# Kernel optimization log

Measured on AMD Instinct MI355X. Metric: run time of the kernel, lower is better.

The kernel has to match this reference:

```python
import jax, jax.numpy as jnp
import numpy as np

B = 256
H, W = 8, 16          # input_resolution for channels=256
C = 768               # dim = channels*3
WS = 4                # window_size
SHIFT = 2             # shift_size
NH = 12               # num_heads
HD = C // NH          # head_dim = 64
HID = 1024            # mlp hidden = channels*4
N = WS * WS           # tokens per window = 16
NW = (H // WS) * (W // WS)  # windows per image = 8
LN_EPS = 1e-5


def _rel_pos_index():
    coords = np.stack(np.meshgrid(np.arange(WS), np.arange(WS), indexing='ij'))  # [2,ws,ws]
    cf = coords.reshape(2, -1)                      # [2, N]
    rel = (cf[:, :, None] - cf[:, None, :]).transpose(1, 2, 0)  # [N, N, 2]
    rel[:, :, 0] += WS - 1
    rel[:, :, 1] += WS - 1
    rel[:, :, 0] *= 2 * WS - 1
    return jnp.asarray(rel.sum(-1))                 # [N, N] int


def _attn_mask():
    img = np.zeros((H, W))
    slices = (slice(0, -WS), slice(-WS, -SHIFT), slice(-SHIFT, None))
    cnt = 0
    for hs in slices:
        for ws_ in slices:
            img[hs, ws_] = cnt
            cnt += 1
    mw = img.reshape(H // WS, WS, W // WS, WS).transpose(0, 2, 1, 3).reshape(-1, N)  # [nW, N]
    am = mw[:, None, :] - mw[:, :, None]            # [nW, N, N]
    return jnp.asarray(np.where(am != 0, -100.0, 0.0).astype(np.float32))


REL_IDX = _rel_pos_index()
ATTN_MASK = _attn_mask()


def _ln(x, g, b):
    m = x.mean(-1, keepdims=True)
    v = ((x - m) ** 2).mean(-1, keepdims=True)
    return (x - m) / jnp.sqrt(v + LN_EPS) * g + b


def setup_inputs() -> dict:
    key = jax.random.key(0)
    ks = jax.random.split(key, 8)
    s = 0.02
    return {
        'x': jax.random.normal(ks[0], (B, H * W, C), jnp.float32),
        'ln1_g': jnp.ones((C,), jnp.float32),
        'ln1_b': jnp.zeros((C,), jnp.float32),
        'qkv_w': jax.random.normal(ks[1], (C, 3 * C), jnp.float32) * s,
        'qkv_b': jnp.zeros((3 * C,), jnp.float32),
        'proj_w': jax.random.normal(ks[2], (C, C), jnp.float32) * s,
        'proj_b': jnp.zeros((C,), jnp.float32),
        'rel_table': jax.random.normal(ks[3], ((2 * WS - 1) * (2 * WS - 1), NH), jnp.float32) * s,
        'ln2_g': jnp.ones((C,), jnp.float32),
        'ln2_b': jnp.zeros((C,), jnp.float32),
        'fc1_w': jax.random.normal(ks[4], (C, HID), jnp.float32) * s,
        'fc1_b': jax.random.normal(ks[5], (HID,), jnp.float32) * 1e-6,
        'fc2_w': jax.random.normal(ks[6], (HID, C), jnp.float32) * s,
        'fc2_b': jax.random.normal(ks[7], (C,), jnp.float32) * 1e-6,
    }


def reference(x, ln1_g, ln1_b, qkv_w, qkv_b, proj_w, proj_b, rel_table,
              ln2_g, ln2_b, fc1_w, fc1_b, fc2_w, fc2_b):
    # --- norm1 + cyclic shift + window partition ---
    h = _ln(x, ln1_g, ln1_b).reshape(B, H, W, C)
    h = jnp.roll(h, (-SHIFT, -SHIFT), axis=(1, 2))
    hw = h.reshape(B, H // WS, WS, W // WS, WS, C).transpose(0, 1, 3, 2, 4, 5)
    hw = hw.reshape(B * NW, N, C)                   # (num_windows*B, N, C)
    # --- window attention with relative position bias + shift mask ---
    qkv = (hw @ qkv_w + qkv_b).reshape(B * NW, N, 3, NH, HD).transpose(2, 0, 3, 1, 4)
    q, k, v = qkv[0] * (HD ** -0.5), qkv[1], qkv[2]  # [Bn, NH, N, HD]
    attn = jnp.einsum('bhnd,bhmd->bhnm', q, k)      # [Bn, NH, N, N]
    bias = rel_table[REL_IDX].transpose(2, 0, 1)    # [NH, N, N]
    attn = attn + bias[None]
    attn = attn.reshape(B, NW, NH, N, N) + ATTN_MASK[None, :, None]
    attn = jax.nn.softmax(attn.reshape(B * NW, NH, N, N), axis=-1)
    o = jnp.einsum('bhnm,bhmd->bhnd', attn, v).transpose(0, 2, 1, 3).reshape(B * NW, N, C)
    o = o @ proj_w + proj_b
    # --- window reverse + reverse shift + residual ---
    o = o.reshape(B, H // WS, W // WS, WS, WS, C).transpose(0, 1, 3, 2, 4, 5).reshape(B, H, W, C)
    o = jnp.roll(o, (SHIFT, SHIFT), axis=(1, 2)).reshape(B, H * W, C)
    x = x + o
    # --- MLP block (dropout is identity at inference) ---
    y = _ln(x, ln2_g, ln2_b)
    y = jax.nn.gelu(y @ fc1_w + fc1_b, approximate=False)
    return x + (y @ fc2_w + fc2_b)
```

## Files before the change

### kernel.cpp

```cpp
#include <hip/hip_runtime.h>
#include <stdint.h>
#include <stddef.h>

typedef __attribute__((ext_vector_type(8))) short bf16x8;
typedef __attribute__((ext_vector_type(4))) float f32x4;
typedef __attribute__((ext_vector_type(4))) unsigned int uint4v;

static __device__ __forceinline__ unsigned short f2bf(float f) {
  unsigned int u = __builtin_bit_cast(unsigned int, f);
  unsigned int r = (u + 0x7FFFu + ((u >> 16) & 1u)) >> 16;
  return (unsigned short)r;
}
static __device__ __forceinline__ float bf2f(unsigned short h) {
  unsigned int u = ((unsigned int)h) << 16;
  return __builtin_bit_cast(float, u);
}
static __device__ __forceinline__ unsigned int pk2(float a, float b) {
  return (unsigned int)f2bf(a) | ((unsigned int)f2bf(b) << 16);
}

static __device__ __forceinline__ void gld16(const void* g, void* l) {
  __builtin_amdgcn_global_load_lds(
      (const __attribute__((address_space(1))) void*)g,
      (__attribute__((address_space(3))) void*)l, 16, 0, 0);
}

__global__ void transpose_cast_all(const float* __restrict__ s0, unsigned short* __restrict__ d0,
                                   const float* __restrict__ s1, unsigned short* __restrict__ d1,
                                   const float* __restrict__ s2, unsigned short* __restrict__ d2,
                                   const float* __restrict__ s3, unsigned short* __restrict__ d3) {
  __shared__ float tile[32][33];
  const int b = blockIdx.x;
  const float* src; unsigned short* dst; int R, C, nbx, bi;
  if (b < 1728)      { src = s0; dst = d0; R = 768;  C = 2304; nbx = 72; bi = b; }
  else if (b < 2304) { src = s1; dst = d1; R = 768;  C = 768;  nbx = 24; bi = b - 1728; }
  else if (b < 3072) { src = s2; dst = d2; R = 768;  C = 1024; nbx = 32; bi = b - 2304; }
  else               { src = s3; dst = d3; R = 1024; C = 768;  nbx = 24; bi = b - 3072; }
  const int bx = bi % nbx, by = bi / nbx;
  const int c0 = bx * 32, r0 = by * 32;
  const int tx = threadIdx.x, ty = threadIdx.y;
  #pragma unroll
  for (int i = 0; i < 32; i += 8)
    tile[ty + i][tx] = src[(size_t)(r0 + ty + i) * C + c0 + tx];
  __syncthreads();
  #pragma unroll
  for (int i = 0; i < 32; i += 8)
    dst[(size_t)(c0 + ty + i) * R + r0 + tx] = f2bf(tile[tx][ty + i]);
}

static __device__ __forceinline__ float blksum256(float v, float* sb) {
  #pragma unroll
  for (int o = 32; o > 0; o >>= 1) v += __shfl_down(v, o, 64);
  int lane = threadIdx.x & 63, w = threadIdx.x >> 6;
  __syncthreads();
  if (lane == 0) sb[w] = v;
  __syncthreads();
  return sb[0] + sb[1] + sb[2] + sb[3];
}

template <int MODE>
__global__ __launch_bounds__(256) void ln_kernel(const float* __restrict__ xf,
                                                 const unsigned short* __restrict__ xb,
                                                 const float* __restrict__ gg,
                                                 const float* __restrict__ bb,
                                                 unsigned short* __restrict__ out) {
  __shared__ float sb[4];
  const int d = blockIdx.x;
  size_t srow;
  if (MODE == 0) {
    int b = d >> 7, wid = (d >> 4) & 7, tok = d & 15;
    int oh = (((wid >> 2) << 2) + (tok >> 2) + 2) & 7;
    int ow = (((wid & 3) << 2) + (tok & 3) + 2) & 15;
    srow = (size_t)(b << 7) + oh * 16 + ow;
  } else {
    srow = d;
  }
  const int t = threadIdx.x;
  const bool ex = t < 128;
  float a0, a1, b0 = 0.f, b1 = 0.f;
  if (MODE == 0) {
    const float2* f2 = (const float2*)(xf + srow * 768);
    float2 p = f2[t]; a0 = p.x; a1 = p.y;
    if (ex) { float2 q = f2[256 + t]; b0 = q.x; b1 = q.y; }
  } else {
    const unsigned int* u = (const unsigned int*)(xb + srow * 768);
    unsigned int p = u[t];
    a0 = bf2f((unsigned short)p); a1 = bf2f((unsigned short)(p >> 16));
    if (ex) {
      unsigned int q = u[256 + t];
      b0 = bf2f((unsigned short)q); b1 = bf2f((unsigned short)(q >> 16));
    }
  }
  float mean = blksum256(a0 + a1 + b0 + b1, sb) * (1.0f / 768.0f);
  float da0 = a0 - mean, da1 = a1 - mean, db0 = b0 - mean, db1 = b1 - mean;
  float var = blksum256(da0 * da0 + da1 * da1 + (ex ? db0 * db0 + db1 * db1 : 0.f), sb) *
              (1.0f / 768.0f);
  float rstd = rsqrtf(var + 1e-5f);
  const float2* g2 = (const float2*)gg;
  const float2* be2 = (const float2*)bb;
  unsigned int* o32 = (unsigned int*)(out + (size_t)d * 768);
  float2 g = g2[t], be = be2[t];
  o32[t] = pk2(da0 * rstd * g.x + be.x, da1 * rstd * g.y + be.y);
  if (ex) {
    float2 gq = g2[256 + t], bq = be2[256 + t];
    o32[256 + t] = pk2(db0 * rstd * gq.x + bq.x, db1 * rstd * gq.y + bq.y);
  }
}

template <int EPI>
__global__ __launch_bounds__(512, 2) void gemm256(
    const unsigned short* __restrict__ A, const unsigned short* __restrict__ BT,
    const float* __restrict__ bias, float* __restrict__ outF,
    unsigned short* __restrict__ outB, const float* __restrict__ resid,
    const unsigned short* __restrict__ residB,
    int M, int N, int K, int NT, int NTILES) {
  __shared__ __align__(16) unsigned short sA[2][256 * 64];
  __shared__ __align__(16) unsigned short sB[2][256 * 64];

  const int tid = threadIdx.x;
  const int lane = tid & 63, wv = tid >> 6;
  const int wr = wv >> 2, wc = wv & 3;
  const int fr = lane & 15, q4 = (lane >> 4) << 2;

  const size_t K2 = (size_t)K * 2;
  const int srow = tid >> 3;
  const int sg = tid & 7;
  const int sgs = ((sg ^ (srow & 7)) << 4);
  char* sdA = (char*)&sA[0][0] + (wv << 10);
  char* sdB = (char*)&sB[0][0] + (wv << 10);

  const int g0 = (((lane >> 4) ^ (fr & 7)) << 4);
  const int g1 = (((4 + (lane >> 4)) ^ (fr & 7)) << 4);
  const int arow = (wr << 7) + fr;
  const int brow = (wc << 6) + fr;

  int v = blockIdx.x;
  if (v >= NTILES) return;
  int sw = (v & 7) * (NTILES >> 3) + (v >> 3);
  int m0 = (sw / NT) << 8, n0 = (sw - (sw / NT) * NT) << 8;
  const char* pA = (const char*)A + (size_t)(m0 + srow) * K2 + sgs;
  const char* pB = (const char*)BT + (size_t)(n0 + srow) * K2 + sgs;
  int vn = v + 256;
  bool more = vn < NTILES;
  int m0n = m0, n0n = n0;
  const char* pAn = pA; const char* pBn = pB;
  if (more) {
    int sw2 = (vn & 7) * (NTILES >> 3) + (vn >> 3);
    m0n = (sw2 / NT) << 8; n0n = (sw2 - (sw2 / NT) * NT) << 8;
    pAn = (const char*)A + (size_t)(m0n + srow) * K2 + sgs;
    pBn = (const char*)BT + (size_t)(n0n + srow) * K2 + sgs;
  }

  f32x4 acc[8][4];
  #pragma unroll
  for (int i = 0; i < 8; ++i)
    #pragma unroll
    for (int j = 0; j < 4; ++j) acc[i][j] = (f32x4){0.f, 0.f, 0.f, 0.f};

  bf16x8 af[4][2];
  bf16x8 bbv[2][2][2];
  const int KT = K >> 6;
  const int NI = KT >> 1;

#define BARR __builtin_amdgcn_s_barrier()
#define LGKM0 asm volatile("s_waitcnt lgkmcnt(0)" ::: "memory")
#define VM6 asm volatile("s_waitcnt vmcnt(6)" ::: "memory")
#define VM0 asm volatile("s_waitcnt vmcnt(0)" ::: "memory")

#define LDA(CB, mh)                                                          \
  {                                                                          \
    const char* ba = ((const char*)&sA[0][0]) + (CB)*32768;                  \
    _Pragma("unroll") for (int fm = 0; fm < 4; ++fm) {                       \
      const int r = arow + (mh)*64 + fm * 16;                                \
      af[fm][0] = *(const bf16x8*)(ba + r * 128 + g0);                       \
      af[fm][1] = *(const bf16x8*)(ba + r * 128 + g1);                       \
    }                                                                        \
  }
#define LDB(CB, nh)                                                          \
  {                                                                          \
    const char* ba = ((const char*)&sB[0][0]) + (CB)*32768;                  \
    _Pragma("unroll") for (int fn = 0; fn < 2; ++fn) {                       \
      const int r = brow + (nh)*32 + fn * 16;                                \
      bbv[nh][fn][0] = *(const bf16x8*)(ba + r * 128 + g0);                  \
      bbv[nh][fn][1] = *(const bf16x8*)(ba + r * 128 + g1);                  \
    }                                                                        \
  }
#define STGA_(P, CB, tt, j)                                                  \
  gld16((P) + (size_t)((j)*64) * K2 + ((size_t)(tt) << 7),                   \
        sdA + (CB)*32768 + (j)*8192);
#define STGB_(P, CB, tt, j)                                                  \
  gld16((P) + (size_t)((j)*64) * K2 + ((size_t)(tt) << 7),                   \
        sdB + (CB)*32768 + (j)*8192);
#define MMAQ(mh, nh)                                                         \
  _Pragma("unroll") for (int fm = 0; fm < 4; ++fm)                           \
      _Pragma("unroll") for (int fn = 0; fn < 2; ++fn) {                     \
    f32x4* ac = &acc[(mh)*4 + fm][(nh)*2 + fn];                              \
    *ac = __builtin_amdgcn_mfma_f32_16x16x32_bf16(af[fm][0], bbv[nh][fn][0], \
                                                  *ac, 0, 0, 0);             \
    *ac = __builtin_amdgcn_mfma_f32_16x16x32_bf16(af[fm][1], bbv[nh][fn][1], \
                                                  *ac, 0, 0, 0);             \
  }
#define OPEN  BARR; LGKM0; __builtin_amdgcn_s_setprio(1)
#define CLOSE __builtin_amdgcn_s_setprio(0)

  #pragma unroll
  for (int j = 0; j < 4; ++j) { STGA_(pA, 0, 0, j); STGB_(pB, 0, 0, j); }
  STGA_(pA, 1, 1, 0); STGA_(pA, 1, 1, 2);
  STGB_(pB, 1, 1, 0); STGB_(pB, 1, 1, 1); STGB_(pB, 1, 1, 2); STGB_(pB, 1, 1, 3);
  VM6;
  BARR;

  for (;;) {
    for (int i = 0; i < NI; ++i) {
      const bool lastit = (i == NI - 1);
      const int s1 = 2 * i + 1;
      const bool gl = (!lastit) || more;
      const char* qA = lastit ? pAn : pA;
      const char* qB = lastit ? pBn : pB;
      const int t2 = lastit ? 0 : 2 * i + 2;
      const int t3 = lastit ? 1 : 2 * i + 3;
      LDB(0, 0) LDA(0, 0)
      STGA_(pA, 1, s1, 1); STGA_(pA, 1, s1, 3);
      OPEN; MMAQ(0, 0); CLOSE; BARR;
      LDB(0, 1)
      if (gl) { STGA_(qA, 0, t2, 0); STGA_(qA, 0, t2, 2); }
      OPEN; MMAQ(0, 1); CLOSE; BARR;
      LDA(0, 1)
      if (gl) { STGB_(qB, 0, t2, 0); STGB_(qB, 0, t2, 1); }
      OPEN; MMAQ(1, 1); CLOSE; BARR;
      if (gl) { STGB_(qB, 0, t2, 2); STGB_(qB, 0, t2, 3); }
      OPEN; MMAQ(1, 0); CLOSE;
      if (gl) { VM6; } else { VM0; }
      BARR;
      LDB(1, 0) LDA(1, 0)
      if (gl) { STGA_(qA, 0, t2, 1); STGA_(qA, 0, t2, 3); }
      OPEN; MMAQ(0, 0); CLOSE; BARR;
      LDB(1, 1)
      if (gl) { STGA_(qA, 1, t3, 0); STGA_(qA, 1, t3, 2); }
      OPEN; MMAQ(0, 1); CLOSE; BARR;
      LDA(1, 1)
      if (gl) { STGB_(qB, 1, t3, 0); STGB_(qB, 1, t3, 1); }
      OPEN; MMAQ(1, 1); CLOSE; BARR;
      if (gl) { STGB_(qB, 1, t3, 2); STGB_(qB, 1, t3, 3); }
      OPEN; MMAQ(1, 0); CLOSE;
      if (gl) { VM6; }
      BARR;
    }

    #pragma unroll
    for (int ai = 0; ai < 8; ++ai) {
      #pragma unroll
      for (int bj = 0; bj < 4; ++bj) {
        const int col = n0 + (wc << 6) + bj * 16 + fr;
        const float bc = bias[col];
        #pragma unroll
        for (int i = 0; i < 4; ++i) {
          const int row = m0 + (wr << 7) + ai * 16 + q4 + i;
          float vvv = acc[ai][bj][i] + bc;
          if (EPI == 0) {
            outB[(size_t)row * N + col] = f2bf(vvv);
          } else if (EPI == 1) {
            int b = row >> 7, wid = (row >> 4) & 7, tok = row & 15;
            int oh = (((wid >> 2) << 2) + (tok >> 2) + 2) & 7;
            int ow = (((wid & 3) << 2) + (tok & 3) + 2) & 15;
            size_t di = ((size_t)(b << 7) + oh * 16 + ow) * 768 + col;
            outB[di] = f2bf(vvv + resid[di]);
          } else if (EPI == 2) {
            float g = 0.5f * vvv * (1.0f + erff(vvv * 0.70710678118f));
            outB[(size_t)row * N + col] = f2bf(g);
          } else {
            size_t di = (size_t)row * N + col;
            outF[di] = vvv + bf2f(residB[di]);
          }
          acc[ai][bj][i] = 0.f;
        }
      }
    }

    v = vn;
    if (v >= NTILES) break;
    pA = pAn; pB = pBn; m0 = m0n; n0 = n0n;
    vn += 256;
    more = (vn < NTILES);
    if (more) {
      int sw2 = (vn & 7) * (NTILES >> 3) + (vn >> 3);
      m0n = (sw2 / NT) << 8; n0n = (sw2 - (sw2 / NT) * NT) << 8;
      pAn = (const char*)A + (size_t)(m0n + srow) * K2 + sgs;
      pBn = (const char*)BT + (size_t)(n0n + srow) * K2 + sgs;
    }
  }
#undef BARR
#undef LGKM0
#undef VM6
#undef VM0
#undef LDA
#undef LDB
#undef STGA_
#undef STGB_
#undef MMAQ
#undef OPEN
#undef CLOSE
}

__global__ __launch_bounds__(64) void attn_win(const unsigned short* __restrict__ qkv,
                                               const float* __restrict__ rel_table,
                                               unsigned short* __restrict__ o) {
  __shared__ __align__(16) unsigned short vt_s[64 * 32];
  __shared__ __align__(16) unsigned short p_s[16 * 32];
  __shared__ __align__(16) unsigned short o_s[16 * 72];
  const int nwg = gridDim.x;
  const int orig = blockIdx.x;
  const int bid = (orig & 7) * (nwg >> 3) + (orig >> 3);
  const int win = bid / 12;
  const int head = bid - win * 12;
  const int wid = win & 7;
  const int lane = threadIdx.x;
  const unsigned short* qb = qkv + (size_t)win * 16 * 2304 + head * 64;
  const int t = lane >> 2, d0 = (lane & 3) << 4;
  unsigned short vv[16];
  *(uint4v*)&vv[0] = *(const uint4v*)(qb + 1536 + (size_t)t * 2304 + d0);
  *(uint4v*)&vv[8] = *(const uint4v*)(qb + 1544 + (size_t)t * 2304 + d0);
  #pragma unroll
  for (int e = 0; e < 16; ++e) vt_s[(d0 + e) * 32 + t] = vv[e];
  #pragma unroll
  for (int e = 0; e < 16; ++e) vt_s[lane * 32 + 16 + e] = 0;
  if (lane < 16) {
    #pragma unroll
    for (int e = 0; e < 16; ++e) p_s[lane * 32 + 16 + e] = 0;
  }
  __syncthreads();

  const int fr = lane & 15, g8 = (lane >> 4) << 3;
  const unsigned short* qrow = qb + (size_t)fr * 2304;
  bf16x8 qa0 = *(const bf16x8*)(qrow + g8);
  bf16x8 qa1 = *(const bf16x8*)(qrow + 32 + g8);
  bf16x8 ka0 = *(const bf16x8*)(qrow + 768 + g8);
  bf16x8 ka1 = *(const bf16x8*)(qrow + 800 + g8);
  f32x4 s = (f32x4){0.f, 0.f, 0.f, 0.f};
  s = __builtin_amdgcn_mfma_f32_16x16x32_bf16(qa0, ka0, s, 0, 0, 0);
  s = __builtin_amdgcn_mfma_f32_16x16x32_bf16(qa1, ka1, s, 0, 0, 0);

  const int wh = wid >> 2, wwc = wid & 3;
  const int rj = fr >> 2, cj = fr & 3;
  const int rowm = wh * 4 + rj, colm = wwc * 4 + cj;
  const int rgm = (rowm < 4 ? 0 : (rowm < 6 ? 1 : 2)) * 3 +
                  (colm < 12 ? 0 : (colm < 14 ? 1 : 2));
  float p[4];
  #pragma unroll
  for (int i = 0; i < 4; ++i) {
    int n = ((lane >> 4) << 2) + i;
    int ri = n >> 2, ci = n & 3;
    int rown = wh * 4 + ri, coln = wwc * 4 + ci;
    int rgn = (rown < 4 ? 0 : (rown < 6 ? 1 : 2)) * 3 +
              (coln < 12 ? 0 : (coln < 14 ? 1 : 2));
    float bias = rel_table[(size_t)((ri - rj + 3) * 7 + (ci - cj + 3)) * 12 + head];
    p[i] = s[i] * 0.125f + bias + (rgn != rgm ? -100.0f : 0.0f);
  }
  float mx[4] = {p[0], p[1], p[2], p[3]};
  #pragma unroll
  for (int off = 8; off > 0; off >>= 1)
    #pragma unroll
    for (int i = 0; i < 4; ++i) mx[i] = fmaxf(mx[i], __shfl_xor(mx[i], off, 64));
  float sm[4];
  #pragma unroll
  for (int i = 0; i < 4; ++i) { p[i] = __expf(p[i] - mx[i]); sm[i] = p[i]; }
  #pragma unroll
  for (int off = 8; off > 0; off >>= 1)
    #pragma unroll
    for (int i = 0; i < 4; ++i) sm[i] += __shfl_xor(sm[i], off, 64);
  #pragma unroll
  for (int i = 0; i < 4; ++i)
    p_s[(((lane >> 4) << 2) + i) * 32 + fr] = f2bf(p[i] / sm[i]);
  __syncthreads();

  bf16x8 pa = *(const bf16x8*)&p_s[fr * 32 + g8];
  const f32x4 oz = (f32x4){0.f, 0.f, 0.f, 0.f};
  #pragma unroll
  for (int c = 0; c < 4; ++c) {
    bf16x8 vb = *(const bf16x8*)&vt_s[(c * 16 + fr) * 32 + g8];
    f32x4 oa = __builtin_amdgcn_mfma_f32_16x16x32_bf16(pa, vb, oz, 0, 0, 0);
    #pragma unroll
    for (int i = 0; i < 4; ++i) {
      int n = ((lane >> 4) << 2) + i;
      o_s[n * 72 + c * 16 + fr] = f2bf(oa[i]);
    }
  }
  __syncthreads();
  const int orow = lane >> 2, oq = lane & 3;
  const unsigned short* srcp = &o_s[orow * 72 + oq * 16];
  unsigned short* dstp = o + ((size_t)win * 16 + orow) * 768 + head * 64 + oq * 16;
  *(uint4v*)dstp = *(const uint4v*)srcp;
  *(uint4v*)(dstp + 8) = *(const uint4v*)(srcp + 8);
}

extern "C" void kernel_launch(void* const* d_in, const int* in_sizes, int n_in,
                              void* d_out, int out_size, void* d_ws, size_t ws_size,
                              hipStream_t stream) {
  const float* x      = (const float*)d_in[0];
  const float* ln1_g  = (const float*)d_in[1];
  const float* ln1_b  = (const float*)d_in[2];
  const float* qkv_w  = (const float*)d_in[3];
  const float* qkv_b  = (const float*)d_in[4];
  const float* proj_w = (const float*)d_in[5];
  const float* proj_b = (const float*)d_in[6];
  const float* rel_t  = (const float*)d_in[7];
  const float* ln2_g  = (const float*)d_in[8];
  const float* ln2_b  = (const float*)d_in[9];
  const float* fc1_w  = (const float*)d_in[10];
  const float* fc1_b  = (const float*)d_in[11];
  const float* fc2_w  = (const float*)d_in[12];
  const float* fc2_b  = (const float*)d_in[13];
  float* out = (float*)d_out;

  char* ws = (char*)d_ws;
  unsigned short* wsA = (unsigned short*)(ws);
  unsigned short* qkvb = (unsigned short*)(ws + 50331648);
  unsigned short* xr16 = (unsigned short*)(ws + 50331648);
  unsigned short* h1 = (unsigned short*)(ws + 201326592);
  unsigned short* qkv_wT = (unsigned short*)(ws + 268435456);
  unsigned short* proj_wT = (unsigned short*)(ws + 271974400);
  unsigned short* fc1_wT = (unsigned short*)(ws + 273154048);
  unsigned short* fc2_wT = (unsigned short*)(ws + 274726912);

  transpose_cast_all<<<3840, dim3(32, 8), 0, stream>>>(qkv_w, qkv_wT, proj_w, proj_wT,
                                                       fc1_w, fc1_wT, fc2_w, fc2_wT);

  ln_kernel<0><<<32768, 256, 0, stream>>>(x, nullptr, ln1_g, ln1_b, wsA);
  gemm256<0><<<256, 512, 0, stream>>>(wsA, qkv_wT, qkv_b, nullptr, qkvb,
                                      nullptr, nullptr,
                                      32768, 2304, 768, 9, 1152);
  attn_win<<<24576, 64, 0, stream>>>(qkvb, rel_t, wsA);
  gemm256<1><<<256, 512, 0, stream>>>(wsA, proj_wT, proj_b, nullptr, xr16,
                                      x, nullptr,
                                      32768, 768, 768, 3, 384);
  ln_kernel<2><<<32768, 256, 0, stream>>>(nullptr, xr16, ln2_g, ln2_b, wsA);
  gemm256<2><<<256, 512, 0, stream>>>(wsA, fc1_wT, fc1_b, nullptr, h1,
                                      nullptr, nullptr,
                                      32768, 1024, 768, 4, 512);
  gemm256<3><<<256, 512, 0, stream>>>(h1, fc2_wT, fc2_b, out, nullptr,
                                      nullptr, xr16,
                                      32768, 768, 1024, 3, 384);
}
```

Measured before the change: 498.6 us.

## Use atomic work-stealing tile scheduler in GEMMs and fuse weight cast with LN1

Persistent GEMM blocks now pick their next tile from a global atomic counter instead of a fixed stride of 256, so faster blocks take more tiles and load stays balanced. The weight transpose-cast kernel and the first LayerNorm are merged into one launch, and a small kernel resets the counters first. This removes one launch and the tail imbalance of the static schedule. It adds an atomic and a block barrier per tile, and the dynamic order can weaken the swizzled L2 locality.

```diff
diff --git a/kernel.cpp b/kernel.cpp
--- a/kernel.cpp
+++ b/kernel.cpp
@@ -25,71 +25,102 @@
       (__attribute__((address_space(3))) void*)l, 16, 0, 0);
 }
 
-__global__ void transpose_cast_all(const float* __restrict__ s0, unsigned short* __restrict__ d0,
-                                   const float* __restrict__ s1, unsigned short* __restrict__ d1,
-                                   const float* __restrict__ s2, unsigned short* __restrict__ d2,
-                                   const float* __restrict__ s3, unsigned short* __restrict__ d3) {
+__global__ void init_ctrs(int* c) {
+  if (threadIdx.x < 4) c[threadIdx.x] = 0;
+}
+
+__global__ __launch_bounds__(256) void fused_pre(
+    const float* __restrict__ s0, unsigned short* __restrict__ d0,
+    const float* __restrict__ s1, unsigned short* __restrict__ d1,
+    const float* __restrict__ s2, unsigned short* __restrict__ d2,
+    const float* __restrict__ s3, unsigned short* __restrict__ d3,
+    const float* __restrict__ x, const float* __restrict__ gg,
+    const float* __restrict__ bb, unsigned short* __restrict__ lnout) {
   __shared__ float tile[32][33];
-  const int b = blockIdx.x;
-  const float* src; unsigned short* dst; int R, C, nbx, bi;
-  if (b < 1728)      { src = s0; dst = d0; R = 768;  C = 2304; nbx = 72; bi = b; }
-  else if (b < 2304) { src = s1; dst = d1; R = 768;  C = 768;  nbx = 24; bi = b - 1728; }
-  else if (b < 3072) { src = s2; dst = d2; R = 768;  C = 1024; nbx = 32; bi = b - 2304; }
-  else               { src = s3; dst = d3; R = 1024; C = 768;  nbx = 24; bi = b - 3072; }
-  const int bx = bi % nbx, by = bi / nbx;
-  const int c0 = bx * 32, r0 = by * 32;
-  const int tx = threadIdx.x, ty = threadIdx.y;
-  #pragma unroll
-  for (int i = 0; i < 32; i += 8)
-    tile[ty + i][tx] = src[(size_t)(r0 + ty + i) * C + c0 + tx];
-  __syncthreads();
-  #pragma unroll
-  for (int i = 0; i < 32; i += 8)
-    dst[(size_t)(c0 + ty + i) * R + r0 + tx] = f2bf(tile[tx][ty + i]);
-}
-
-static __device__ __forceinline__ float blksum256(float v, float* sb) {
-  #pragma unroll
-  for (int o = 32; o > 0; o >>= 1) v += __shfl_down(v, o, 64);
-  int lane = threadIdx.x & 63, w = threadIdx.x >> 6;
-  __syncthreads();
-  if (lane == 0) sb[w] = v;
-  __syncthreads();
-  return sb[0] + sb[1] + sb[2] + sb[3];
-}
-
-template <int MODE>
-__global__ __launch_bounds__(256) void ln_kernel(const float* __restrict__ xf,
-                                                 const unsigned short* __restrict__ xb,
-                                                 const float* __restrict__ gg,
-                                                 const float* __restrict__ bb,
-                                                 unsigned short* __restrict__ out) {
-  __shared__ float sb[4];
-  const int d = blockIdx.x;
-  size_t srow;
-  if (MODE == 0) {
-    int b = d >> 7, wid = (d >> 4) & 7, tok = d & 15;
-    int oh = (((wid >> 2) << 2) + (tok >> 2) + 2) & 7;
-    int ow = (((wid & 3) << 2) + (tok & 3) + 2) & 15;
-    srow = (size_t)(b << 7) + oh * 16 + ow;
-  } else {
-    srow = d;
-  }
+  const int blk = blockIdx.x;
+  if (blk < 3840) {
+    const float* src; unsigned short* dst; int R, C, nbx, bi;
+    if (blk < 1728)      { src = s0; dst = d0; R = 768;  C = 2304; nbx = 72; bi = blk; }
+    else if (blk < 2304) { src = s1; dst = d1; R = 768;  C = 768;  nbx = 24; bi = blk - 1728; }
+    else if (blk < 3072) { src = s2; dst = d2; R = 768;  C = 1024; nbx = 32; bi = blk - 2304; }
+    else                 { src = s3; dst = d3; R = 1024; C = 768;  nbx = 24; bi = blk - 3072; }
+    const int bx = bi % nbx, by = bi / nbx;
+    const int c0 = bx * 32, r0 = by * 32;
+    const int tx = threadIdx.x & 31, ty = threadIdx.x >> 5;
+    #pragma unroll
+    for (int i = 0; i < 32; i += 8)
+      tile[ty + i][tx] = src[(size_t)(r0 + ty + i) * C + c0 + tx];
+    __syncthreads();
+    #pragma unroll
+    for (int i = 0; i < 32; i += 8)
+      dst[(size_t)(c0 + ty + i) * R + r0 + tx] = f2bf(tile[tx][ty + i]);
+    return;
+  }
+  float* sb = &tile[0][0];
+  const int d = blk - 3840;
+  int b = d >> 7, wid = (d >> 4) & 7, tok = d & 15;
+  int oh = (((wid >> 2) << 2) + (tok >> 2) + 2) & 7;
+  int ow = (((wid & 3) << 2) + (tok & 3) + 2) & 15;
+  size_t srow = (size_t)(b << 7) + oh * 16 + ow;
   const int t = threadIdx.x;
   const bool ex = t < 128;
   float a0, a1, b0 = 0.f, b1 = 0.f;
-  if (MODE == 0) {
-    const float2* f2 = (const float2*)(xf + srow * 768);
-    float2 p = f2[t]; a0 = p.x; a1 = p.y;
-    if (ex) { float2 q = f2[256 + t]; b0 = q.x; b1 = q.y; }
-  } else {
-    const unsigned int* u = (const unsigned int*)(xb + srow * 768);
-    unsigned int p = u[t];
-    a0 = bf2f((unsigned short)p); a1 = bf2f((unsigned short)(p >> 16));
-    if (ex) {
-      unsigned int q = u[256 + t];
-      b0 = bf2f((unsigned short)q); b1 = bf2f((unsigned short)(q >> 16));
-    }
+  const float2* f2 = (const float2*)(x + srow * 768);
+  float2 p = f2[t]; a0 = p.x; a1 = p.y;
+  if (ex) { float2 q = f2[256 + t]; b0 = q.x; b1 = q.y; }
+  float v = a0 + a1 + b0 + b1;
+  #pragma unroll
+  for (int o = 32; o > 0; o >>= 1) v += __shfl_down(v, o, 64);
+  int lane = t & 63, w = t >> 6;
+  __syncthreads();
+  if (lane == 0) sb[w] = v;
+  __syncthreads();
+  float mean = (sb[0] + sb[1] + sb[2] + sb[3]) * (1.0f / 768.0f);
+  float da0 = a0 - mean, da1 = a1 - mean, db0 = b0 - mean, db1 = b1 - mean;
+  float vv = da0 * da0 + da1 * da1 + (ex ? db0 * db0 + db1 * db1 : 0.f);
+  #pragma unroll
+  for (int o = 32; o > 0; o >>= 1) vv += __shfl_down(vv, o, 64);
+  __syncthreads();
+  if (lane == 0) sb[w] = vv;
+  __syncthreads();
+  float var = (sb[0] + sb[1] + sb[2] + sb[3]) * (1.0f / 768.0f);
+  float rstd = rsqrtf(var + 1e-5f);
+  const float2* g2 = (const float2*)gg;
+  const float2* be2 = (const float2*)bb;
+  unsigned int* o32 = (unsigned int*)(lnout + (size_t)d * 768);
+  float2 g = g2[t], be = be2[t];
+  o32[t] = pk2(da0 * rstd * g.x + be.x, da1 * rstd * g.y + be.y);
+  if (ex) {
+    float2 gq = g2[256 + t], bq = be2[256 + t];
+    o32[256 + t] = pk2(db0 * rstd * gq.x + bq.x, db1 * rstd * gq.y + bq.y);
+  }
+}
+
+static __device__ __forceinline__ float blksum256(float v, float* sb) {
+  #pragma unroll
+  for (int o = 32; o > 0; o >>= 1) v += __shfl_down(v, o, 64);
+  int lane = threadIdx.x & 63, w = threadIdx.x >> 6;
+  __syncthreads();
+  if (lane == 0) sb[w] = v;
+  __syncthreads();
+  return sb[0] + sb[1] + sb[2] + sb[3];
+}
+
+__global__ __launch_bounds__(256) void ln2_kernel(const unsigned short* __restrict__ xb,
+                                                  const float* __restrict__ gg,
+                                                  const float* __restrict__ bb,
+                                                  unsigned short* __restrict__ out) {
+  __shared__ float sb[4];
+  const int d = blockIdx.x;
+  const int t = threadIdx.x;
+  const bool ex = t < 128;
+  float a0, a1, b0 = 0.f, b1 = 0.f;
+  const unsigned int* u = (const unsigned int*)(xb + (size_t)d * 768);
+  unsigned int p = u[t];
+  a0 = bf2f((unsigned short)p); a1 = bf2f((unsigned short)(p >> 16));
+  if (ex) {
+    unsigned int q = u[256 + t];
+    b0 = bf2f((unsigned short)q); b1 = bf2f((unsigned short)(q >> 16));
   }
   float mean = blksum256(a0 + a1 + b0 + b1, sb) * (1.0f / 768.0f);
   float da0 = a0 - mean, da1 = a1 - mean, db0 = b0 - mean, db1 = b1 - mean;
@@ -113,9 +144,10 @@
     const float* __restrict__ bias, float* __restrict__ outF,
     unsigned short* __restrict__ outB, const float* __restrict__ resid,
     const unsigned short* __restrict__ residB,
-    int M, int N, int K, int NT, int NTILES) {
+    int M, int N, int K, int NT, int NTILES, int* __restrict__ ctr) {
   __shared__ __align__(16) unsigned short sA[2][256 * 64];
   __shared__ __align__(16) unsigned short sB[2][256 * 64];
+  __shared__ int sh_vn;
 
   const int tid = threadIdx.x;
   const int lane = tid & 63, wv = tid >> 6;
@@ -135,12 +167,13 @@
   const int brow = (wc << 6) + fr;
 
   int v = blockIdx.x;
-  if (v >= NTILES) return;
   int sw = (v & 7) * (NTILES >> 3) + (v >> 3);
   int m0 = (sw / NT) << 8, n0 = (sw - (sw / NT) * NT) << 8;
   const char* pA = (const char*)A + (size_t)(m0 + srow) * K2 + sgs;
   const char* pB = (const char*)BT + (size_t)(n0 + srow) * K2 + sgs;
-  int vn = v + 256;
+  if (tid == 0) sh_vn = 256 + atomicAdd(ctr, 1);
+  __syncthreads();
+  int vn = sh_vn;
   bool more = vn < NTILES;
   int m0n = m0, n0n = n0;
   const char* pAn = pA; const char* pBn = pB;
@@ -277,10 +310,12 @@
       }
     }
 
+    if (!more) break;
     v = vn;
-    if (v >= NTILES) break;
     pA = pAn; pB = pBn; m0 = m0n; n0 = n0n;
-    vn += 256;
+    if (tid == 0) sh_vn = 256 + atomicAdd(ctr, 1);
+    __syncthreads();
+    vn = sh_vn;
     more = (vn < NTILES);
     if (more) {
       int sw2 = (vn & 7) * (NTILES >> 3) + (vn >> 3);
@@ -421,23 +456,25 @@
   unsigned short* proj_wT = (unsigned short*)(ws + 271974400);
   unsigned short* fc1_wT = (unsigned short*)(ws + 273154048);
   unsigned short* fc2_wT = (unsigned short*)(ws + 274726912);
-
-  transpose_cast_all<<<3840, dim3(32, 8), 0, stream>>>(qkv_w, qkv_wT, proj_w, proj_wT,
-                                                       fc1_w, fc1_wT, fc2_w, fc2_wT);
-
-  ln_kernel<0><<<32768, 256, 0, stream>>>(x, nullptr, ln1_g, ln1_b, wsA);
+  int* ctrs = (int*)(ws + 276299776);
+
+  init_ctrs<<<1, 64, 0, stream>>>(ctrs);
+  fused_pre<<<36608, 256, 0, stream>>>(qkv_w, qkv_wT, proj_w, proj_wT,
+                                       fc1_w, fc1_wT, fc2_w, fc2_wT,
+                                       x, ln1_g, ln1_b, wsA);
+
   gemm256<0><<<256, 512, 0, stream>>>(wsA, qkv_wT, qkv_b, nullptr, qkvb,
                                       nullptr, nullptr,
-                                      32768, 2304, 768, 9, 1152);
+                                      32768, 2304, 768, 9, 1152, ctrs + 0);
   attn_win<<<24576, 64, 0, stream>>>(qkvb, rel_t, wsA);
   gemm256<1><<<256, 512, 0, stream>>>(wsA, proj_wT, proj_b, nullptr, xr16,
                                       x, nullptr,
-                                      32768, 768, 768, 3, 384);
-  ln_kernel<2><<<32768, 256, 0, stream>>>(nullptr, xr16, ln2_g, ln2_b, wsA);
+                                      32768, 768, 768, 3, 384, ctrs + 1);
+  ln2_kernel<<<32768, 256, 0, stream>>>(xr16, ln2_g, ln2_b, wsA);
   gemm256<2><<<256, 512, 0, stream>>>(wsA, fc1_wT, fc1_b, nullptr, h1,
                                       nullptr, nullptr,
-                                      32768, 1024, 768, 4, 512);
+                                      32768, 1024, 768, 4, 512, ctrs + 2);
   gemm256<3><<<256, 512, 0, stream>>>(h1, fc2_wT, fc2_b, out, nullptr,
                                       nullptr, xr16,
-                                      32768, 768, 1024, 3, 384);
-}
+                                      32768, 768, 1024, 3, 384, ctrs + 3);
+}
```

After: 516.6 us. 3.6% more time.
